# Performance work log

Measured on AMD Instinct MI355X. Metric: run time of the kernel, lower is better.

## Reference

```python
import jax, jax.numpy as jnp
import numpy as np

B, D = 8192, 1024            # batch, inputs_dim
H1, H2, H3 = 2048, 1024, 512 # expert_units
NS, NT = 8, 4                # num_shared_experts, num_tasks_experts
E = NS + 3 * NT              # 20 experts total: [shared 0:8 | SA 8:12 | RA 12:16 | EA 16:20]
TU1, TU2 = 1024, 512         # tower_units
TIN = H3 * 4                 # tower input dim = 2048


def lrelu(x):
    return jnp.where(x >= 0, x, 0.1 * x)


def setup_inputs() -> dict:
    key = jax.random.key(0)
    ks = jax.random.split(key, 24)
    s = 0.02
    return {
        "inputs": jax.random.normal(ks[0], (B, D), jnp.float32),
        # stacked expert MLP params (leading axis = expert index)
        "W1": jax.random.normal(ks[1], (E, D, H1), jnp.float32) * s,
        "b1": jnp.zeros((E, H1), jnp.float32),
        "W2": jax.random.normal(ks[2], (E, H1, H2), jnp.float32) * s,
        "b2": jnp.zeros((E, H2), jnp.float32),
        "W3": jax.random.normal(ks[3], (E, H2, H3), jnp.float32) * s,
        "b3": jnp.zeros((E, H3), jnp.float32),
        # gate linears (single layer + softmax over dim 1)
        "Wg_sh": jax.random.normal(ks[4], (D, NS + 3 * NT), jnp.float32) * s,
        "bg_sh": jnp.zeros((NS + 3 * NT,), jnp.float32),
        "Wg_sa": jax.random.normal(ks[5], (D, NT + NS), jnp.float32) * s,
        "bg_sa": jnp.zeros((NT + NS,), jnp.float32),
        "Wg_ra": jax.random.normal(ks[6], (D, NT + NS), jnp.float32) * s,
        "bg_ra": jnp.zeros((NT + NS,), jnp.float32),
        "Wg_ea": jax.random.normal(ks[7], (D, NT + NS), jnp.float32) * s,
        "bg_ea": jnp.zeros((NT + NS,), jnp.float32),
        # 2 towers (one per task), stacked on leading axis
        "Wt1": jax.random.normal(ks[8], (2, TIN, TU1), jnp.float32) * s,
        "bt1": jnp.zeros((2, TU1), jnp.float32),
        "Wt2": jax.random.normal(ks[9], (2, TU1, TU2), jnp.float32) * s,
        "bt2": jnp.zeros((2, TU2), jnp.float32),
        # per-task output denses: PRESENCE=6, AIRFLOW=4
        "Wd0": jax.random.normal(ks[10], (TU2, 6), jnp.float32) * s,
        "bd0": jnp.zeros((6,), jnp.float32),
        "Wd1": jax.random.normal(ks[11], (TU2, 4), jnp.float32) * s,
        "bd1": jnp.zeros((4,), jnp.float32),
    }


def reference(inputs, W1, b1, W2, b2, W3, b3,
              Wg_sh, bg_sh, Wg_sa, bg_sa, Wg_ra, bg_ra, Wg_ea, bg_ea,
              Wt1, bt1, Wt2, bt2, Wd0, bd0, Wd1, bd1):
    x = inputs
    # all 20 experts as batched GEMMs: [E, B, h]
    h = lrelu(jnp.einsum('bd,edh->ebh', x, W1) + b1[:, None, :])
    h = lrelu(jnp.einsum('ebh,ehk->ebk', h, W2) + b2[:, None, :])
    eo = lrelu(jnp.einsum('ebk,eko->ebo', h, W3) + b3[:, None, :])  # [E,B,H3]

    # gates (softmax over feature dim)
    g_sh = jax.nn.softmax(x @ Wg_sh + bg_sh, axis=1)  # [B, 20]
    g_sa = jax.nn.softmax(x @ Wg_sa + bg_sa, axis=1)  # [B, 12]
    g_ra = jax.nn.softmax(x @ Wg_ra + bg_ra, axis=1)
    g_ea = jax.nn.softmax(x @ Wg_ea + bg_ea, axis=1)

    # shared gate: order = shared + SA + RA + EA == natural stacking order
    out_sh = jnp.einsum('ebh,be->bh', eo, g_sh)
    # task gates: order = task experts + shared experts
    out_sa = jnp.einsum('ebh,be->bh', jnp.concatenate([eo[NS:NS+NT], eo[:NS]], 0), g_sa)
    out_ra = jnp.einsum('ebh,be->bh', jnp.concatenate([eo[NS+NT:NS+2*NT], eo[:NS]], 0), g_ra)
    out_ea = jnp.einsum('ebh,be->bh', jnp.concatenate([eo[NS+2*NT:], eo[:NS]], 0), g_ea)

    tower_in = jnp.concatenate([out_sh, out_sa, out_ra, out_ea], axis=1)  # [B, 2048]
    t = lrelu(jnp.einsum('bi,kio->kbo', tower_in, Wt1) + bt1[:, None, :])  # [2,B,TU1]
    t = lrelu(jnp.einsum('kbo,kop->kbp', t, Wt2) + bt2[:, None, :])        # [2,B,TU2]
    out0 = t[0] @ Wd0 + bd0  # [B, 6]  PRESENCE
    out1 = t[1] @ Wd1 + bd1  # [B, 4]  AIRFLOW
    return (out0, out1)
```

## Files before the change

kernel.cpp:

```cpp
#include <hip/hip_runtime.h>

#define DEV __device__ __forceinline__

typedef __bf16 bf16x8 __attribute__((ext_vector_type(8)));
typedef float f32x4 __attribute__((ext_vector_type(4)));

DEV unsigned short f2bf(float f) {
  union { float f; unsigned u; } v; v.f = f;
  unsigned r = v.u + 0x7FFFu + ((v.u >> 16) & 1u);
  return (unsigned short)(r >> 16);
}
DEV float bf2f(unsigned short h) {
  union { float f; unsigned u; } v; v.u = ((unsigned)h) << 16;
  return v.f;
}

DEV void gload16(const void* g, void* l) {
  __builtin_amdgcn_global_load_lds(
      (__attribute__((address_space(1))) void*)(g),
      (__attribute__((address_space(3))) void*)(l), 16, 0, 0);
}

#define MFMA16(a, b, c) __builtin_amdgcn_mfma_f32_16x16x32_bf16((a), (b), (c), 0, 0, 0)

DEV void gemm256_body(
    const unsigned short* __restrict__ A,
    const unsigned short* __restrict__ Bt,
    const float* __restrict__ bias,
    unsigned short* __restrict__ Out,
    int K, int lda, int ldo, int nbx, int nby,
    long sA, long sB, long sBias, long sOut,
    int bid, int nwg)
{
  int wg = bid;
  {
    const int q = nwg >> 3, r = nwg & 7;
    const int xcd = wg & 7, pos = wg >> 3;
    wg = (xcd < r ? xcd * (q + 1) : r * (q + 1) + (xcd - r) * q) + pos;
  }
  const int per_z = nbx * nby;
  const int z  = wg / per_z;
  const int rz = wg - z * per_z;
  const int by = rz / nbx;
  const int bx = rz - by * nbx;

  A    += (size_t)z * sA;
  Bt   += (size_t)z * sB;
  bias += (size_t)z * sBias;
  Out  += (size_t)z * sOut;

  const int tid  = threadIdx.x;
  const int lane = tid & 63;
  const int wid  = tid >> 6;
  const int wm   = wid >> 2, wn = wid & 3;
  const int m0   = by * 256, n0 = bx * 256;

  __shared__ alignas(16) char sm[2][65536];

  f32x4 acc[8][4];
  const f32x4 fz = {0.f, 0.f, 0.f, 0.f};
#pragma unroll
  for (int i = 0; i < 8; ++i)
#pragma unroll
    for (int j = 0; j < 4; ++j) acc[i][j] = fz;

  const int rr = tid >> 3;
  const int ch = (tid & 7) ^ (rr & 7);
  const char* gA = (const char*)A  + ((size_t)(m0 + rr) * lda) * 2 + ch * 16;
  const char* gB = (const char*)Bt + ((size_t)(n0 + rr) * K)   * 2 + ch * 16;
  const size_t stepA = (size_t)64 * lda * 2;
  const size_t stepB = (size_t)64 * K * 2;

  const int koff0 = (((lane >> 4) << 4) ^ ((lane & 7) << 4));
  const int aRow  = wm * 128 + (lane & 15);
  const int bRow  = wn * 64  + (lane & 15);

  const int nkt = K >> 6;

  auto SA = [&](int buf, int kt, int jh) {
    const char* s = gA + (size_t)kt * 128 + (2 * jh) * stepA;
    char* l = sm[buf] + tid * 16 + (2 * jh) * 8192;
    gload16(s, l);
    gload16(s + stepA, l + 8192);
  };
  auto SB = [&](int buf, int kt, int jh) {
    const char* s = gB + (size_t)kt * 128 + (2 * jh) * stepB;
    char* l = sm[buf] + 32768 + tid * 16 + (2 * jh) * 8192;
    gload16(s, l);
    gload16(s + stepB, l + 8192);
  };

  SA(0, 0, 0); SA(0, 0, 1); SB(0, 0, 0); SB(0, 0, 1);

  for (int kt = 0; kt < nkt; ++kt) {
    const int cur = kt & 1, nb = cur ^ 1;
    const bool pre = (kt + 1 < nkt);
    if (pre) {
      SA(nb, kt + 1, 0);
      asm volatile("s_waitcnt vmcnt(2)" ::: "memory");
    } else {
      asm volatile("s_waitcnt vmcnt(0)" ::: "memory");
    }
    __builtin_amdgcn_s_barrier();
    __builtin_amdgcn_sched_barrier(0);

    const char* pA = sm[cur] + aRow * 128;
    const char* pB = sm[cur] + 32768 + bRow * 128;
    bf16x8 a0[4], a1[4], b0[4], b1[4];

    {
#pragma unroll
      for (int i = 0; i < 4; ++i) a0[i] = *(const bf16x8*)(pA + i * 2048 + koff0);
#pragma unroll
      for (int n = 0; n < 4; ++n) b0[n] = *(const bf16x8*)(pB + n * 2048 + koff0);
      if (pre) SA(nb, kt + 1, 1);
      asm volatile("s_waitcnt lgkmcnt(0)" ::: "memory");
      __builtin_amdgcn_sched_barrier(0);
      __builtin_amdgcn_s_setprio(1);
#pragma unroll
      for (int i = 0; i < 4; ++i)
#pragma unroll
        for (int n = 0; n < 4; ++n) acc[i][n] = MFMA16(a0[i], b0[n], acc[i][n]);
      __builtin_amdgcn_s_setprio(0);
      __builtin_amdgcn_sched_barrier(0);
      __builtin_amdgcn_s_barrier();
      __builtin_amdgcn_sched_barrier(0);
    }
    {
#pragma unroll
      for (int i = 0; i < 4; ++i) a1[i] = *(const bf16x8*)(pA + (i + 4) * 2048 + koff0);
      if (pre) { SB(nb, kt + 1, 0); SB(nb, kt + 1, 1); }
      asm volatile("s_waitcnt lgkmcnt(0)" ::: "memory");
      __builtin_amdgcn_sched_barrier(0);
      __builtin_amdgcn_s_setprio(1);
#pragma unroll
      for (int i = 0; i < 4; ++i)
#pragma unroll
        for (int n = 0; n < 4; ++n) acc[i + 4][n] = MFMA16(a1[i], b0[n], acc[i + 4][n]);
      __builtin_amdgcn_s_setprio(0);
      __builtin_amdgcn_sched_barrier(0);
      __builtin_amdgcn_s_barrier();
      __builtin_amdgcn_sched_barrier(0);
    }
    {
      const int ko = koff0 ^ 64;
#pragma unroll
      for (int i = 0; i < 4; ++i) a0[i] = *(const bf16x8*)(pA + i * 2048 + ko);
#pragma unroll
      for (int n = 0; n < 4; ++n) b1[n] = *(const bf16x8*)(pB + n * 2048 + ko);
      asm volatile("s_waitcnt lgkmcnt(0)" ::: "memory");
      __builtin_amdgcn_sched_barrier(0);
      __builtin_amdgcn_s_setprio(1);
#pragma unroll
      for (int i = 0; i < 4; ++i)
#pragma unroll
        for (int n = 0; n < 4; ++n) acc[i][n] = MFMA16(a0[i], b1[n], acc[i][n]);
      __builtin_amdgcn_s_setprio(0);
      __builtin_amdgcn_sched_barrier(0);
      __builtin_amdgcn_s_barrier();
      __builtin_amdgcn_sched_barrier(0);
    }
    {
      const int ko = koff0 ^ 64;
#pragma unroll
      for (int i = 0; i < 4; ++i) a1[i] = *(const bf16x8*)(pA + (i + 4) * 2048 + ko);
      asm volatile("s_waitcnt lgkmcnt(0)" ::: "memory");
      __builtin_amdgcn_sched_barrier(0);
      __builtin_amdgcn_s_setprio(1);
#pragma unroll
      for (int i = 0; i < 4; ++i)
#pragma unroll
        for (int n = 0; n < 4; ++n) acc[i + 4][n] = MFMA16(a1[i], b1[n], acc[i + 4][n]);
      __builtin_amdgcn_s_setprio(0);
      __builtin_amdgcn_sched_barrier(0);
      __builtin_amdgcn_s_barrier();
      __builtin_amdgcn_sched_barrier(0);
    }
  }

#pragma unroll
  for (int ni = 0; ni < 4; ++ni) {
    const int c = n0 + wn * 64 + ni * 16 + (lane & 15);
    const float bv = bias[c];
#pragma unroll
    for (int mi = 0; mi < 8; ++mi) {
      const int r0 = m0 + wm * 128 + mi * 16 + ((lane >> 4) << 2);
#pragma unroll
      for (int j = 0; j < 4; ++j) {
        float v = acc[mi][ni][j] + bv;
        v = v >= 0.f ? v : 0.1f * v;
        Out[(size_t)(r0 + j) * ldo + c] = f2bf(v);
      }
    }
  }
}

__global__ __launch_bounds__(512) void gemm_dual(
    const unsigned short* A1, const unsigned short* Bt1, const float* bias1,
    unsigned short* O1, int K1, int lda1, int ldo1, int nbx1, int nby1,
    long sA1, long sB1, long sBias1, long sO1,
    const unsigned short* A2, const unsigned short* Bt2, const float* bias2,
    unsigned short* O2, int K2, int lda2, int ldo2, int nbx2, int nby2,
    long sA2, long sB2, long sBias2, long sO2,
    int split)
{
  const bool one = ((int)blockIdx.x < split);
  const unsigned short* A  = one ? A1 : A2;
  const unsigned short* Bt = one ? Bt1 : Bt2;
  const float* bias        = one ? bias1 : bias2;
  unsigned short* Out      = one ? O1 : O2;
  const int K   = one ? K1 : K2;
  const int lda = one ? lda1 : lda2;
  const int ldo = one ? ldo1 : ldo2;
  const int nbx = one ? nbx1 : nbx2;
  const int nby = one ? nby1 : nby2;
  const long sA = one ? sA1 : sA2;
  const long sB = one ? sB1 : sB2;
  const long sBias = one ? sBias1 : sBias2;
  const long sOut  = one ? sO1 : sO2;
  const int bid = one ? (int)blockIdx.x : (int)blockIdx.x - split;
  const int nwg = one ? split : (int)gridDim.x - split;
  gemm256_body(A, Bt, bias, Out, K, lda, ldo, nbx, nby, sA, sB, sBias, sOut,
               bid, nwg);
}

#define GEMM_DEF(NAME)                                                        \
__global__ __launch_bounds__(512) void NAME(                                  \
    const unsigned short* __restrict__ A,                                     \
    const unsigned short* __restrict__ Bt,                                    \
    const float* __restrict__ bias,                                           \
    unsigned short* __restrict__ Out,                                         \
    int K, int lda, int ldo, int nbx, int nby,                                \
    long sA, long sB, long sBias, long sOut) {                                \
  gemm256_body(A, Bt, bias, Out, K, lda, ldo, nbx, nby, sA, sB, sBias, sOut,  \
               (int)blockIdx.x, (int)gridDim.x);                              \
}
GEMM_DEF(gemm_l3)
GEMM_DEF(gemm_tw)

DEV float gateW(const float* Wsh, const float* Wsa, const float* Wra,
                const float* Wea, int k, int c) {
  if (c < 20) return Wsh[(size_t)k * 20 + c];
  if (c < 32) return Wsa[(size_t)k * 12 + (c - 20)];
  if (c < 44) return Wra[(size_t)k * 12 + (c - 32)];
  if (c < 56) return Wea[(size_t)k * 12 + (c - 44)];
  return 0.f;
}
DEV float gateB(const float* bsh, const float* bsa, const float* bra,
                const float* bea, int c) {
  if (c < 20) return bsh[c];
  if (c < 32) return bsa[c - 20];
  if (c < 44) return bra[c - 32];
  if (c < 56) return bea[c - 44];
  return 0.f;
}

__global__ __launch_bounds__(256) void prep_all(
    const float* __restrict__ W1,  const float* __restrict__ W2,
    const float* __restrict__ W3,  const float* __restrict__ Wt1,
    const float* __restrict__ Wt2, const float* __restrict__ x,
    const float* __restrict__ Wsh, const float* __restrict__ bsh,
    const float* __restrict__ Wsa, const float* __restrict__ bsa,
    const float* __restrict__ Wra, const float* __restrict__ bra,
    const float* __restrict__ Wea, const float* __restrict__ bea,
    unsigned short* __restrict__ W1t,  unsigned short* __restrict__ W2t,
    unsigned short* __restrict__ W3t,  unsigned short* __restrict__ Wt1t,
    unsigned short* __restrict__ Wt2t, unsigned short* __restrict__ xb,
    float* __restrict__ logits)
{
  const int id = blockIdx.x;
  const int t  = threadIdx.x;

  if (id < 128) {
    __shared__ alignas(16) float smg[4096];
    float (*sx)[64] = (float (*)[64])smg;
    float (*sw)[64] = (float (*)[64])(smg + 2048);
    const int b0 = id * 64;
    const int tr = t >> 4, tc = t & 15;
    float acc[4][4] = {};

    for (int kt = 0; kt < 32; ++kt) {
      const int k0 = kt * 32;
      __syncthreads();
#pragma unroll
      for (int it = 0; it < 2; ++it) {
        const int idx = t + it * 256;
        const int r = idx >> 3, c4 = (idx & 7) * 4;
        const float4 v = *(const float4*)(x + (size_t)(b0 + r) * 1024 + k0 + c4);
        sx[c4 + 0][r] = v.x; sx[c4 + 1][r] = v.y;
        sx[c4 + 2][r] = v.z; sx[c4 + 3][r] = v.w;
      }
#pragma unroll
      for (int it = 0; it < 2; ++it) {
        const int idx = t + it * 256;
        const int row = idx >> 4;
        const int c4  = (idx & 15) * 4;
#pragma unroll
        for (int j = 0; j < 4; ++j)
          sw[row][c4 + j] = gateW(Wsh, Wsa, Wra, Wea, k0 + row, c4 + j);
      }
      __syncthreads();
#pragma unroll
      for (int kk = 0; kk < 32; ++kk) {
        const float4 rx = *(const float4*)&sx[kk][tr * 4];
        const float4 wv = *(const float4*)&sw[kk][tc * 4];
#pragma unroll
        for (int i = 0; i < 4; ++i) {
          const float xv = (i == 0) ? rx.x : (i == 1) ? rx.y : (i == 2) ? rx.z : rx.w;
          acc[i][0] += xv * wv.x; acc[i][1] += xv * wv.y;
          acc[i][2] += xv * wv.z; acc[i][3] += xv * wv.w;
        }
      }
    }
    float bv[4];
#pragma unroll
    for (int j = 0; j < 4; ++j) bv[j] = gateB(bsh, bsa, bra, bea, tc * 4 + j);
#pragma unroll
    for (int i = 0; i < 4; ++i) {
      float4 o;
      o.x = acc[i][0] + bv[0]; o.y = acc[i][1] + bv[1];
      o.z = acc[i][2] + bv[2]; o.w = acc[i][3] + bv[3];
      *(float4*)&logits[(size_t)(b0 + tr * 4 + i) * 64 + tc * 4] = o;
    }
    return;
  }

  if (id >= 24448) {
    const int local = id - 24448;
    const int r0 = (local >> 4) * 64, c0 = (local & 15) * 64;
#pragma unroll
    for (int i = 0; i < 4; ++i) {
      const int row = r0 + i * 16 + (t >> 4);
      const int col = c0 + (t & 15) * 4;
      const float4 v = *(const float4*)(x + (size_t)row * 1024 + col);
      ushort4 u = make_ushort4(f2bf(v.x), f2bf(v.y), f2bf(v.z), f2bf(v.w));
      *(ushort4*)(xb + (size_t)row * 1024 + col) = u;
    }
    return;
  }

  const int g = id - 128;
  const float* src; unsigned short* dst; int K, N, local;
  if (g < 10240)      { src = W1;  dst = W1t;  K = 1024; N = 2048; local = g; }
  else if (g < 20480) { src = W2;  dst = W2t;  K = 2048; N = 1024; local = g - 10240; }
  else if (g < 23040) { src = W3;  dst = W3t;  K = 1024; N = 512;  local = g - 20480; }
  else if (g < 24064) { src = Wt1; dst = Wt1t; K = 2048; N = 1024; local = g - 23040; }
  else                { src = Wt2; dst = Wt2t; K = 1024; N = 512;  local = g - 24064; }

  const int nkt = K >> 6, nnt = N >> 6;
  const int per_z = nkt * nnt;
  const int z   = local / per_z;
  const int rem = local - z * per_z;
  const int k0  = (rem % nkt) * 64;
  const int n0  = (rem / nkt) * 64;
  src += (size_t)z * K * N;
  dst += (size_t)z * K * N;

  const int i4 = (t >> 4) * 4;
  const int j4 = (t & 15) * 4;
  float a[4][4];
#pragma unroll
  for (int rr = 0; rr < 4; ++rr)
    *(float4*)a[rr] = *(const float4*)(src + (size_t)(k0 + i4 + rr) * N + n0 + j4);
#pragma unroll
  for (int c = 0; c < 4; ++c) {
    ushort4 u = make_ushort4(f2bf(a[0][c]), f2bf(a[1][c]),
                             f2bf(a[2][c]), f2bf(a[3][c]));
    *(ushort4*)(dst + (size_t)(n0 + j4 + c) * K + k0 + i4) = u;
  }
}

__global__ __launch_bounds__(256) void combine_k(
    const unsigned short* __restrict__ eo,
    const float* __restrict__ logits,
    unsigned short* __restrict__ tin)
{
  const int b = blockIdx.x;
  const int t = threadIdx.x;
  __shared__ alignas(16) unsigned short lds[20][512];
  __shared__ float gsm[56];
  const unsigned short* er = eo + (size_t)b * 10240;
  unsigned short* ldsf = &lds[0][0];
#pragma unroll
  for (int i = 0; i < 5; ++i)
    gload16(er + (i * 256 + t) * 8, ldsf + (i * 256 + t) * 8);

  if (t < 64) {
    const float v0 = (t < 56) ? logits[(size_t)b * 64 + t] : 0.f;
    const int off[4] = {0, 20, 32, 44};
    const int wd[4]  = {20, 12, 12, 12};
    for (int g = 0; g < 4; ++g) {
      const bool in = (t >= off[g]) && (t < off[g] + wd[g]);
      float vv = in ? v0 : -1e30f;
      float m = vv;
#pragma unroll
      for (int o = 32; o; o >>= 1) m = fmaxf(m, __shfl_xor(m, o));
      float e = in ? __expf(vv - m) : 0.f;
      float s = e;
#pragma unroll
      for (int o = 32; o; o >>= 1) s += __shfl_xor(s, o);
      if (in) gsm[t] = e / s;
    }
  }
  __syncthreads();

  const int sec = t >> 6;
  const int h0 = (t & 63) * 8;
  float acc[8] = {0.f, 0.f, 0.f, 0.f, 0.f, 0.f, 0.f, 0.f};
  if (sec == 0) {
    for (int e = 0; e < 20; ++e) {
      const float w = gsm[e];
#pragma unroll
      for (int j = 0; j < 8; ++j) acc[j] += w * bf2f(lds[e][h0 + j]);
    }
  } else {
    const int goff = 20 + (sec - 1) * 12;
    const int ebase = 8 + (sec - 1) * 4;
    for (int tt = 0; tt < 4; ++tt) {
      const float w = gsm[goff + tt];
#pragma unroll
      for (int j = 0; j < 8; ++j) acc[j] += w * bf2f(lds[ebase + tt][h0 + j]);
    }
    for (int ss = 0; ss < 8; ++ss) {
      const float w = gsm[goff + 4 + ss];
#pragma unroll
      for (int j = 0; j < 8; ++j) acc[j] += w * bf2f(lds[ss][h0 + j]);
    }
  }
  unsigned short* ob = tin + (size_t)b * 2048 + sec * 512 + h0;
  ushort4 u0 = make_ushort4(f2bf(acc[0]), f2bf(acc[1]), f2bf(acc[2]), f2bf(acc[3]));
  ushort4 u1 = make_ushort4(f2bf(acc[4]), f2bf(acc[5]), f2bf(acc[6]), f2bf(acc[7]));
  *(ushort4*)ob = u0;
  *(ushort4*)(ob + 4) = u1;
}

__global__ __launch_bounds__(256) void outd_k(
    const unsigned short* __restrict__ t2,
    const float* __restrict__ Wd0, const float* __restrict__ bd0,
    const float* __restrict__ Wd1, const float* __restrict__ bd1,
    float* __restrict__ out)
{
  const int gid = blockIdx.x * 4 + (threadIdx.x >> 6);
  const int lane = threadIdx.x & 63;
  const int b = gid >> 1, task = gid & 1;
  const uint4 raw = *(const uint4*)(t2 + ((size_t)task * 8192 + b) * 512 + lane * 8);
  const unsigned short* rs = (const unsigned short*)&raw;
  float v[8];
#pragma unroll
  for (int j = 0; j < 8; ++j) v[j] = bf2f(rs[j]);
  const float* Wd = task ? Wd1 : Wd0;
  const float* bd = task ? bd1 : bd0;
  const int ncol = task ? 4 : 6;
  float* ob = task ? (out + (size_t)8192 * 6 + (size_t)b * 4) : (out + (size_t)b * 6);
  for (int c = 0; c < ncol; ++c) {
    float p = 0.f;
#pragma unroll
    for (int j = 0; j < 8; ++j) p += v[j] * Wd[(size_t)(lane * 8 + j) * ncol + c];
#pragma unroll
    for (int o = 32; o; o >>= 1) p += __shfl_xor(p, o);
    if (lane == 0) ob[c] = p + bd[c];
  }
}

extern "C" void kernel_launch(void* const* d_in, const int* in_sizes, int n_in,
                              void* d_out, int out_size, void* d_ws, size_t ws_size,
                              hipStream_t stream) {
  const float* x     = (const float*)d_in[0];
  const float* W1    = (const float*)d_in[1];
  const float* b1    = (const float*)d_in[2];
  const float* W2    = (const float*)d_in[3];
  const float* b2    = (const float*)d_in[4];
  const float* W3    = (const float*)d_in[5];
  const float* b3    = (const float*)d_in[6];
  const float* Wg_sh = (const float*)d_in[7];
  const float* bg_sh = (const float*)d_in[8];
  const float* Wg_sa = (const float*)d_in[9];
  const float* bg_sa = (const float*)d_in[10];
  const float* Wg_ra = (const float*)d_in[11];
  const float* bg_ra = (const float*)d_in[12];
  const float* Wg_ea = (const float*)d_in[13];
  const float* bg_ea = (const float*)d_in[14];
  const float* Wt1   = (const float*)d_in[15];
  const float* bt1   = (const float*)d_in[16];
  const float* Wt2   = (const float*)d_in[17];
  const float* bt2   = (const float*)d_in[18];
  const float* Wd0   = (const float*)d_in[19];
  const float* bd0   = (const float*)d_in[20];
  const float* Wd1   = (const float*)d_in[21];
  const float* bd1   = (const float*)d_in[22];
  float* out = (float*)d_out;

  const int B = 8192, D = 1024, H1 = 2048, H2 = 1024, H3 = 512;
  const int E = 20, TU1 = 1024, TU2 = 512, TIN = 2048;

  auto rnd = [](size_t n) { return (n + 255) & ~(size_t)255; };
  const size_t szTin = rnd((size_t)B * TIN * 2);
  const size_t szT1  = rnd((size_t)2 * B * TU1 * 2);
  const size_t szH1e = rnd((size_t)B * H1 * 2);
  const size_t szH2e = rnd((size_t)B * H2 * 2);

  char* w = (char*)d_ws;
  auto alloc = [&](size_t n) { char* p = w; w += rnd(n); return p; };
  unsigned short* xb   = (unsigned short*)alloc((size_t)B * D * 2);
  unsigned short* W1t  = (unsigned short*)alloc((size_t)E * H1 * D * 2);
  unsigned short* W2t  = (unsigned short*)alloc((size_t)E * H2 * H1 * 2);
  unsigned short* W3t  = (unsigned short*)alloc((size_t)E * H3 * H2 * 2);
  unsigned short* Wt1t = (unsigned short*)alloc((size_t)2 * TU1 * TIN * 2);
  unsigned short* Wt2t = (unsigned short*)alloc((size_t)2 * TU2 * TU1 * 2);
  float*          lgts = (float*)alloc((size_t)B * 64 * 4);
  unsigned short* eo   = (unsigned short*)alloc((size_t)E * B * H3 * 2);
  char* hreg = w;
  unsigned short* h1  = (unsigned short*)hreg;
  unsigned short* h2  = (unsigned short*)(hreg + 4 * szH1e);
  unsigned short* tin = (unsigned short*)hreg;
  unsigned short* t1  = (unsigned short*)(hreg + szTin);
  unsigned short* t2  = (unsigned short*)(hreg + szTin + szT1);
  (void)in_sizes; (void)n_in; (void)out_size; (void)ws_size;

  prep_all<<<dim3(26496), 256, 0, stream>>>(
      W1, W2, W3, Wt1, Wt2, x,
      Wg_sh, bg_sh, Wg_sa, bg_sa, Wg_ra, bg_ra, Wg_ea, bg_ea,
      W1t, W2t, W3t, Wt1t, Wt2t, xb, lgts);

  for (int k = 0; k <= 10; ++k) {
    const bool has1 = (k < 10), has2 = (k > 0);
    const int split = has1 ? 512 : 0;
    const int total = split + (has2 ? 256 : 0);
    const int p1 = k, p2 = k - 1;
    const unsigned short* A1 = xb;
    const unsigned short* B1 = W1t + (size_t)(2 * (has1 ? p1 : 0)) * H1 * D;
    const float* bb1 = b1 + (size_t)(2 * (has1 ? p1 : 0)) * H1;
    unsigned short* O1 = h1 + (size_t)((has1 ? p1 : 0) & 1) * 2 * B * H1;
    const unsigned short* A2 = h1 + (size_t)((has2 ? p2 : 0) & 1) * 2 * B * H1;
    const unsigned short* B2 = W2t + (size_t)(2 * (has2 ? p2 : 0)) * H2 * H1;
    const float* bb2 = b2 + (size_t)(2 * (has2 ? p2 : 0)) * H2;
    unsigned short* O2 = h2 + (size_t)((2 * (has2 ? p2 : 0)) & 3) * B * H2;
    gemm_dual<<<dim3(total), 512, 0, stream>>>(
        A1, B1, bb1, O1, D, D, H1, H1 / 256, B / 256,
        0, (long)H1 * D, (long)H1, (long)B * H1,
        A2, B2, bb2, O2, H1, H1, H2, H2 / 256, B / 256,
        (long)B * H1, (long)H2 * H1, (long)H2, (long)B * H2,
        split);
    if (k >= 2 && (k & 1) == 0) {
      const int w2 = (k - 2) / 2;
      gemm_l3<<<dim3((H3 / 256) * (B / 256) * 4), 512, 0, stream>>>(
          h2, W3t + (size_t)(4 * w2) * H3 * H2, b3 + (size_t)(4 * w2) * H3,
          eo + (size_t)(4 * w2) * H3,
          H2, H2, E * H3, H3 / 256, B / 256,
          (long)B * H2, (long)H3 * H2, (long)H3, (long)H3);
    }
  }

  combine_k<<<dim3(B), 256, 0, stream>>>(eo, lgts, tin);

  gemm_tw<<<dim3((TU1 / 256) * (B / 256) * 2), 512, 0, stream>>>(
      tin, Wt1t, bt1, t1, TIN, TIN, TU1, TU1 / 256, B / 256,
      0, (long)TU1 * TIN, (long)TU1, (long)B * TU1);
  gemm_tw<<<dim3((TU2 / 256) * (B / 256) * 2), 512, 0, stream>>>(
      t1, Wt2t, bt2, t2, TU1, TU1, TU2, TU2 / 256, B / 256,
      (long)B * TU1, (long)TU2 * TU1, (long)TU2, (long)B * TU2);

  outd_k<<<dim3(B * 2 / 4), 256, 0, stream>>>(t2, Wd0, bd0, Wd1, bd1, out);
}
```

Baseline: 2.064 ms.

## Make GEMM kernels persistent and prefetch next tile's first stage during epilogue

Turns the 256x256 GEMM body into a persistent loop: the grid is capped at 256 workgroups (one per CU) and each workgroup walks tiles with stride gridDim. The first k-stage of the next tile is loaded into LDS before the current tile's epilogue stores, so that load latency hides behind the output writes. This removes per-workgroup launch and prologue cost and tail effects, but changes the XCD tile-swizzle mapping because tile indices are now decoded per iteration. It also adds serialization within each CU, since a second workgroup can no longer co-reside to hide stalls.

After: 2.047 ms. No clear change (-0.8%).

```diff
diff --git a/kernel.cpp b/kernel.cpp
--- a/kernel.cpp
+++ b/kernel.cpp
@@ -23,14 +23,19 @@
 
 #define MFMA16(a, b, c) __builtin_amdgcn_mfma_f32_16x16x32_bf16((a), (b), (c), 0, 0, 0)
 
-DEV void gemm256_body(
-    const unsigned short* __restrict__ A,
-    const unsigned short* __restrict__ Bt,
-    const float* __restrict__ bias,
-    unsigned short* __restrict__ Out,
-    int K, int lda, int ldo, int nbx, int nby,
-    long sA, long sB, long sBias, long sOut,
-    int bid, int nwg)
+struct TileCtx {
+  const char* gA;
+  const char* gB;
+  size_t stepA, stepB;
+  const float* bias;
+  unsigned short* Out;
+  int nkt, ldo, n0, m0;
+};
+
+DEV TileCtx tile_decode(int bid, int nwg,
+    const unsigned short* A, const unsigned short* Bt, const float* bias,
+    unsigned short* Out, int K, int lda, int ldo, int nbx, int nby,
+    long sA, long sB, long sBias, long sOut, int rr, int ch)
 {
   int wg = bid;
   {
@@ -44,154 +49,190 @@
   const int by = rz / nbx;
   const int bx = rz - by * nbx;
 
-  A    += (size_t)z * sA;
-  Bt   += (size_t)z * sB;
-  bias += (size_t)z * sBias;
-  Out  += (size_t)z * sOut;
+  TileCtx c;
+  c.nkt = K >> 6;
+  c.ldo = ldo;
+  c.m0  = by * 256;
+  c.n0  = bx * 256;
+  c.bias = bias + (size_t)z * sBias;
+  c.Out  = Out  + (size_t)z * sOut;
+  c.gA = (const char*)(A  + (size_t)z * sA) + ((size_t)(c.m0 + rr) * lda) * 2 + ch * 16;
+  c.gB = (const char*)(Bt + (size_t)z * sB) + ((size_t)(c.n0 + rr) * K)   * 2 + ch * 16;
+  c.stepA = (size_t)64 * lda * 2;
+  c.stepB = (size_t)64 * K * 2;
+  return c;
+}
+
+DEV void gemm_persist(
+    const unsigned short* A1, const unsigned short* Bt1, const float* bias1,
+    unsigned short* O1, int K1, int lda1, int ldo1, int nbx1, int nby1,
+    long sA1, long sB1, long sBias1, long sO1,
+    const unsigned short* A2, const unsigned short* Bt2, const float* bias2,
+    unsigned short* O2, int K2, int lda2, int ldo2, int nbx2, int nby2,
+    long sA2, long sB2, long sBias2, long sO2,
+    int split, int total)
+{
+  __shared__ alignas(16) char sm[2][65536];
+  char* smb = &sm[0][0];
 
   const int tid  = threadIdx.x;
   const int lane = tid & 63;
   const int wid  = tid >> 6;
   const int wm   = wid >> 2, wn = wid & 3;
-  const int m0   = by * 256, n0 = bx * 256;
-
-  __shared__ alignas(16) char sm[2][65536];
-
-  f32x4 acc[8][4];
-  const f32x4 fz = {0.f, 0.f, 0.f, 0.f};
-#pragma unroll
-  for (int i = 0; i < 8; ++i)
-#pragma unroll
-    for (int j = 0; j < 4; ++j) acc[i][j] = fz;
-
   const int rr = tid >> 3;
   const int ch = (tid & 7) ^ (rr & 7);
-  const char* gA = (const char*)A  + ((size_t)(m0 + rr) * lda) * 2 + ch * 16;
-  const char* gB = (const char*)Bt + ((size_t)(n0 + rr) * K)   * 2 + ch * 16;
-  const size_t stepA = (size_t)64 * lda * 2;
-  const size_t stepB = (size_t)64 * K * 2;
-
   const int koff0 = (((lane >> 4) << 4) ^ ((lane & 7) << 4));
   const int aRow  = wm * 128 + (lane & 15);
   const int bRow  = wn * 64  + (lane & 15);
 
-  const int nkt = K >> 6;
-
-  auto SA = [&](int buf, int kt, int jh) {
-    const char* s = gA + (size_t)kt * 128 + (2 * jh) * stepA;
-    char* l = sm[buf] + tid * 16 + (2 * jh) * 8192;
+  auto dec = [&](int tix) -> TileCtx {
+    if (tix < split)
+      return tile_decode(tix, split, A1, Bt1, bias1, O1, K1, lda1, ldo1,
+                         nbx1, nby1, sA1, sB1, sBias1, sO1, rr, ch);
+    return tile_decode(tix - split, total - split, A2, Bt2, bias2, O2, K2,
+                       lda2, ldo2, nbx2, nby2, sA2, sB2, sBias2, sO2, rr, ch);
+  };
+  auto SA = [&](const TileCtx& c, int buf, int kt, int jh) {
+    const char* s = c.gA + (size_t)kt * 128 + (2 * jh) * c.stepA;
+    char* l = smb + buf * 65536 + tid * 16 + (2 * jh) * 8192;
     gload16(s, l);
-    gload16(s + stepA, l + 8192);
+    gload16(s + c.stepA, l + 8192);
   };
-  auto SB = [&](int buf, int kt, int jh) {
-    const char* s = gB + (size_t)kt * 128 + (2 * jh) * stepB;
-    char* l = sm[buf] + 32768 + tid * 16 + (2 * jh) * 8192;
+  auto SB = [&](const TileCtx& c, int buf, int kt, int jh) {
+    const char* s = c.gB + (size_t)kt * 128 + (2 * jh) * c.stepB;
+    char* l = smb + buf * 65536 + 32768 + tid * 16 + (2 * jh) * 8192;
     gload16(s, l);
-    gload16(s + stepB, l + 8192);
+    gload16(s + c.stepB, l + 8192);
   };
-
-  SA(0, 0, 0); SA(0, 0, 1); SB(0, 0, 0); SB(0, 0, 1);
-
-  for (int kt = 0; kt < nkt; ++kt) {
-    const int cur = kt & 1, nb = cur ^ 1;
-    const bool pre = (kt + 1 < nkt);
-    if (pre) {
-      SA(nb, kt + 1, 0);
-      asm volatile("s_waitcnt vmcnt(2)" ::: "memory");
-    } else {
-      asm volatile("s_waitcnt vmcnt(0)" ::: "memory");
-    }
-    __builtin_amdgcn_s_barrier();
-    __builtin_amdgcn_sched_barrier(0);
-
-    const char* pA = sm[cur] + aRow * 128;
-    const char* pB = sm[cur] + 32768 + bRow * 128;
-    bf16x8 a0[4], a1[4], b0[4], b1[4];
-
-    {
-#pragma unroll
-      for (int i = 0; i < 4; ++i) a0[i] = *(const bf16x8*)(pA + i * 2048 + koff0);
-#pragma unroll
-      for (int n = 0; n < 4; ++n) b0[n] = *(const bf16x8*)(pB + n * 2048 + koff0);
-      if (pre) SA(nb, kt + 1, 1);
-      asm volatile("s_waitcnt lgkmcnt(0)" ::: "memory");
-      __builtin_amdgcn_sched_barrier(0);
-      __builtin_amdgcn_s_setprio(1);
-#pragma unroll
-      for (int i = 0; i < 4; ++i)
-#pragma unroll
-        for (int n = 0; n < 4; ++n) acc[i][n] = MFMA16(a0[i], b0[n], acc[i][n]);
-      __builtin_amdgcn_s_setprio(0);
-      __builtin_amdgcn_sched_barrier(0);
+  auto STAGE0 = [&](const TileCtx& c) {
+    SA(c, 0, 0, 0); SA(c, 0, 0, 1); SB(c, 0, 0, 0); SB(c, 0, 0, 1);
+  };
+
+  int tix = (int)blockIdx.x;
+  if (tix >= total) return;
+  TileCtx cur = dec(tix);
+  STAGE0(cur);
+
+  f32x4 acc[8][4];
+  const f32x4 fz = {0.f, 0.f, 0.f, 0.f};
+
+  while (true) {
+#pragma unroll
+    for (int i = 0; i < 8; ++i)
+#pragma unroll
+      for (int j = 0; j < 4; ++j) acc[i][j] = fz;
+
+    const int nkt = cur.nkt;
+    for (int kt = 0; kt < nkt; ++kt) {
+      const int cb = kt & 1, nb = cb ^ 1;
+      const bool pre = (kt + 1 < nkt);
+      if (pre) {
+        SA(cur, nb, kt + 1, 0);
+        asm volatile("s_waitcnt vmcnt(2)" ::: "memory");
+      } else {
+        asm volatile("s_waitcnt vmcnt(0)" ::: "memory");
+      }
       __builtin_amdgcn_s_barrier();
       __builtin_amdgcn_sched_barrier(0);
-    }
-    {
-#pragma unroll
-      for (int i = 0; i < 4; ++i) a1[i] = *(const bf16x8*)(pA + (i + 4) * 2048 + koff0);
-      if (pre) { SB(nb, kt + 1, 0); SB(nb, kt + 1, 1); }
-      asm volatile("s_waitcnt lgkmcnt(0)" ::: "memory");
-      __builtin_amdgcn_sched_barrier(0);
-      __builtin_amdgcn_s_setprio(1);
-#pragma unroll
-      for (int i = 0; i < 4; ++i)
-#pragma unroll
-        for (int n = 0; n < 4; ++n) acc[i + 4][n] = MFMA16(a1[i], b0[n], acc[i + 4][n]);
-      __builtin_amdgcn_s_setprio(0);
-      __builtin_amdgcn_sched_barrier(0);
-      __builtin_amdgcn_s_barrier();
-      __builtin_amdgcn_sched_barrier(0);
-    }
-    {
-      const int ko = koff0 ^ 64;
-#pragma unroll
-      for (int i = 0; i < 4; ++i) a0[i] = *(const bf16x8*)(pA + i * 2048 + ko);
-#pragma unroll
-      for (int n = 0; n < 4; ++n) b1[n] = *(const bf16x8*)(pB + n * 2048 + ko);
-      asm volatile("s_waitcnt lgkmcnt(0)" ::: "memory");
-      __builtin_amdgcn_sched_barrier(0);
-      __builtin_amdgcn_s_setprio(1);
-#pragma unroll
-      for (int i = 0; i < 4; ++i)
-#pragma unroll
-        for (int n = 0; n < 4; ++n) acc[i][n] = MFMA16(a0[i], b1[n], acc[i][n]);
-      __builtin_amdgcn_s_setprio(0);
-      __builtin_amdgcn_sched_barrier(0);
-      __builtin_amdgcn_s_barrier();
-      __builtin_amdgcn_sched_barrier(0);
-    }
-    {
-      const int ko = koff0 ^ 64;
-#pragma unroll
-      for (int i = 0; i < 4; ++i) a1[i] = *(const bf16x8*)(pA + (i + 4) * 2048 + ko);
-      asm volatile("s_waitcnt lgkmcnt(0)" ::: "memory");
-      __builtin_amdgcn_sched_barrier(0);
-      __builtin_amdgcn_s_setprio(1);
-#pragma unroll
-      for (int i = 0; i < 4; ++i)
-#pragma unroll
-        for (int n = 0; n < 4; ++n) acc[i + 4][n] = MFMA16(a1[i], b1[n], acc[i + 4][n]);
-      __builtin_amdgcn_s_setprio(0);
-      __builtin_amdgcn_sched_barrier(0);
-      __builtin_amdgcn_s_barrier();
-      __builtin_amdgcn_sched_barrier(0);
-    }
-  }
-
-#pragma unroll
-  for (int ni = 0; ni < 4; ++ni) {
-    const int c = n0 + wn * 64 + ni * 16 + (lane & 15);
-    const float bv = bias[c];
-#pragma unroll
-    for (int mi = 0; mi < 8; ++mi) {
-      const int r0 = m0 + wm * 128 + mi * 16 + ((lane >> 4) << 2);
-#pragma unroll
-      for (int j = 0; j < 4; ++j) {
-        float v = acc[mi][ni][j] + bv;
-        v = v >= 0.f ? v : 0.1f * v;
-        Out[(size_t)(r0 + j) * ldo + c] = f2bf(v);
-      }
-    }
+
+      const char* pA = smb + cb * 65536 + aRow * 128;
+      const char* pB = smb + cb * 65536 + 32768 + bRow * 128;
+      bf16x8 a0[4], a1[4], b0[4], b1[4];
+
+      {
+#pragma unroll
+        for (int i = 0; i < 4; ++i) a0[i] = *(const bf16x8*)(pA + i * 2048 + koff0);
+#pragma unroll
+        for (int n = 0; n < 4; ++n) b0[n] = *(const bf16x8*)(pB + n * 2048 + koff0);
+        if (pre) SA(cur, nb, kt + 1, 1);
+        asm volatile("s_waitcnt lgkmcnt(0)" ::: "memory");
+        __builtin_amdgcn_sched_barrier(0);
+        __builtin_amdgcn_s_setprio(1);
+#pragma unroll
+        for (int i = 0; i < 4; ++i)
+#pragma unroll
+          for (int n = 0; n < 4; ++n) acc[i][n] = MFMA16(a0[i], b0[n], acc[i][n]);
+        __builtin_amdgcn_s_setprio(0);
+        __builtin_amdgcn_sched_barrier(0);
+        __builtin_amdgcn_s_barrier();
+        __builtin_amdgcn_sched_barrier(0);
+      }
+      {
+#pragma unroll
+        for (int i = 0; i < 4; ++i) a1[i] = *(const bf16x8*)(pA + (i + 4) * 2048 + koff0);
+        if (pre) { SB(cur, nb, kt + 1, 0); SB(cur, nb, kt + 1, 1); }
+        asm volatile("s_waitcnt lgkmcnt(0)" ::: "memory");
+        __builtin_amdgcn_sched_barrier(0);
+        __builtin_amdgcn_s_setprio(1);
+#pragma unroll
+        for (int i = 0; i < 4; ++i)
+#pragma unroll
+          for (int n = 0; n < 4; ++n) acc[i + 4][n] = MFMA16(a1[i], b0[n], acc[i + 4][n]);
+        __builtin_amdgcn_s_setprio(0);
+        __builtin_amdgcn_sched_barrier(0);
+        __builtin_amdgcn_s_barrier();
+        __builtin_amdgcn_sched_barrier(0);
+      }
+      {
+        const int ko = koff0 ^ 64;
+#pragma unroll
+        for (int i = 0; i < 4; ++i) a0[i] = *(const bf16x8*)(pA + i * 2048 + ko);
+#pragma unroll
+        for (int n = 0; n < 4; ++n) b1[n] = *(const bf16x8*)(pB + n * 2048 + ko);
+        asm volatile("s_waitcnt lgkmcnt(0)" ::: "memory");
+        __builtin_amdgcn_sched_barrier(0);
+        __builtin_amdgcn_s_setprio(1);
+#pragma unroll
+        for (int i = 0; i < 4; ++i)
+#pragma unroll
+          for (int n = 0; n < 4; ++n) acc[i][n] = MFMA16(a0[i], b1[n], acc[i][n]);
+        __builtin_amdgcn_s_setprio(0);
+        __builtin_amdgcn_sched_barrier(0);
+        __builtin_amdgcn_s_barrier();
+        __builtin_amdgcn_sched_barrier(0);
+      }
+      {
+        const int ko = koff0 ^ 64;
+#pragma unroll
+        for (int i = 0; i < 4; ++i) a1[i] = *(const bf16x8*)(pA + (i + 4) * 2048 + ko);
+        asm volatile("s_waitcnt lgkmcnt(0)" ::: "memory");
+        __builtin_amdgcn_sched_barrier(0);
+        __builtin_amdgcn_s_setprio(1);
+#pragma unroll
+        for (int i = 0; i < 4; ++i)
+#pragma unroll
+          for (int n = 0; n < 4; ++n) acc[i + 4][n] = MFMA16(a1[i], b1[n], acc[i + 4][n]);
+        __builtin_amdgcn_s_setprio(0);
+        __builtin_amdgcn_sched_barrier(0);
+        __builtin_amdgcn_s_barrier();
+        __builtin_amdgcn_sched_barrier(0);
+      }
+    }
+
+    const int nxt = tix + (int)gridDim.x;
+    const bool has = nxt < total;
+    TileCtx nc;
+    if (has) { nc = dec(nxt); STAGE0(nc); }
+
+#pragma unroll
+    for (int ni = 0; ni < 4; ++ni) {
+      const int c = cur.n0 + wn * 64 + ni * 16 + (lane & 15);
+      const float bv = cur.bias[c];
+#pragma unroll
+      for (int mi = 0; mi < 8; ++mi) {
+        const int r0 = cur.m0 + wm * 128 + mi * 16 + ((lane >> 4) << 2);
+#pragma unroll
+        for (int j = 0; j < 4; ++j) {
+          float v = acc[mi][ni][j] + bv;
+          v = v >= 0.f ? v : 0.1f * v;
+          cur.Out[(size_t)(r0 + j) * cur.ldo + c] = f2bf(v);
+        }
+      }
+    }
+
+    if (!has) return;
+    cur = nc;
+    tix = nxt;
   }
 }
 
@@ -202,38 +243,22 @@
     const unsigned short* A2, const unsigned short* Bt2, const float* bias2,
     unsigned short* O2, int K2, int lda2, int ldo2, int nbx2, int nby2,
     long sA2, long sB2, long sBias2, long sO2,
-    int split)
+    int split, int total)
 {
-  const bool one = ((int)blockIdx.x < split);
-  const unsigned short* A  = one ? A1 : A2;
-  const unsigned short* Bt = one ? Bt1 : Bt2;
-  const float* bias        = one ? bias1 : bias2;
-  unsigned short* Out      = one ? O1 : O2;
-  const int K   = one ? K1 : K2;
-  const int lda = one ? lda1 : lda2;
-  const int ldo = one ? ldo1 : ldo2;
-  const int nbx = one ? nbx1 : nbx2;
-  const int nby = one ? nby1 : nby2;
-  const long sA = one ? sA1 : sA2;
-  const long sB = one ? sB1 : sB2;
-  const long sBias = one ? sBias1 : sBias2;
-  const long sOut  = one ? sO1 : sO2;
-  const int bid = one ? (int)blockIdx.x : (int)blockIdx.x - split;
-  const int nwg = one ? split : (int)gridDim.x - split;
-  gemm256_body(A, Bt, bias, Out, K, lda, ldo, nbx, nby, sA, sB, sBias, sOut,
-               bid, nwg);
+  gemm_persist(A1, Bt1, bias1, O1, K1, lda1, ldo1, nbx1, nby1,
+               sA1, sB1, sBias1, sO1,
+               A2, Bt2, bias2, O2, K2, lda2, ldo2, nbx2, nby2,
+               sA2, sB2, sBias2, sO2, split, total);
 }
 
 #define GEMM_DEF(NAME)                                                        \
 __global__ __launch_bounds__(512) void NAME(                                  \
-    const unsigned short* __restrict__ A,                                     \
-    const unsigned short* __restrict__ Bt,                                    \
-    const float* __restrict__ bias,                                           \
-    unsigned short* __restrict__ Out,                                         \
-    int K, int lda, int ldo, int nbx, int nby,                                \
-    long sA, long sB, long sBias, long sOut) {                                \
-  gemm256_body(A, Bt, bias, Out, K, lda, ldo, nbx, nby, sA, sB, sBias, sOut,  \
-               (int)blockIdx.x, (int)gridDim.x);                              \
+    const unsigned short* A, const unsigned short* Bt, const float* bias,     \
+    unsigned short* Out, int K, int lda, int ldo, int nbx, int nby,           \
+    long sA, long sB, long sBias, long sOut, int total) {                     \
+  gemm_persist(A, Bt, bias, Out, K, lda, ldo, nbx, nby, sA, sB, sBias, sOut,  \
+               A, Bt, bias, Out, K, lda, ldo, nbx, nby, sA, sB, sBias, sOut,  \
+               total, total);                                                 \
 }
 GEMM_DEF(gemm_l3)
 GEMM_DEF(gemm_tw)
@@ -497,7 +522,6 @@
   const size_t szTin = rnd((size_t)B * TIN * 2);
   const size_t szT1  = rnd((size_t)2 * B * TU1 * 2);
   const size_t szH1e = rnd((size_t)B * H1 * 2);
-  const size_t szH2e = rnd((size_t)B * H2 * 2);
 
   char* w = (char*)d_ws;
   auto alloc = [&](size_t n) { char* p = w; w += rnd(n); return p; };
@@ -535,30 +559,31 @@
     const unsigned short* B2 = W2t + (size_t)(2 * (has2 ? p2 : 0)) * H2 * H1;
     const float* bb2 = b2 + (size_t)(2 * (has2 ? p2 : 0)) * H2;
     unsigned short* O2 = h2 + (size_t)((2 * (has2 ? p2 : 0)) & 3) * B * H2;
-    gemm_dual<<<dim3(total), 512, 0, stream>>>(
+    const int grid = total < 256 ? total : 256;
+    gemm_dual<<<dim3(grid), 512, 0, stream>>>(
         A1, B1, bb1, O1, D, D, H1, H1 / 256, B / 256,
         0, (long)H1 * D, (long)H1, (long)B * H1,
         A2, B2, bb2, O2, H1, H1, H2, H2 / 256, B / 256,
         (long)B * H1, (long)H2 * H1, (long)H2, (long)B * H2,
-        split);
+        split, total);
     if (k >= 2 && (k & 1) == 0) {
       const int w2 = (k - 2) / 2;
-      gemm_l3<<<dim3((H3 / 256) * (B / 256) * 4), 512, 0, stream>>>(
+      gemm_l3<<<dim3(256), 512, 0, stream>>>(
           h2, W3t + (size_t)(4 * w2) * H3 * H2, b3 + (size_t)(4 * w2) * H3,
           eo + (size_t)(4 * w2) * H3,
           H2, H2, E * H3, H3 / 256, B / 256,
-          (long)B * H2, (long)H3 * H2, (long)H3, (long)H3);
+          (long)B * H2, (long)H3 * H2, (long)H3, (long)H3, 256);
     }
   }
 
   combine_k<<<dim3(B), 256, 0, stream>>>(eo, lgts, tin);
 
-  gemm_tw<<<dim3((TU1 / 256) * (B / 256) * 2), 512, 0, stream>>>(
+  gemm_tw<<<dim3(256), 512, 0, stream>>>(
       tin, Wt1t, bt1, t1, TIN, TIN, TU1, TU1 / 256, B / 256,
-      0, (long)TU1 * TIN, (long)TU1, (long)B * TU1);
-  gemm_tw<<<dim3((TU2 / 256) * (B / 256) * 2), 512, 0, stream>>>(
+      0, (long)TU1 * TIN, (long)TU1, (long)B * TU1, 256);
+  gemm_tw<<<dim3(128), 512, 0, stream>>>(
       t1, Wt2t, bt2, t2, TU1, TU1, TU2, TU2 / 256, B / 256,
-      (long)B * TU1, (long)TU2 * TU1, (long)TU2, (long)B * TU2);
+      (long)B * TU1, (long)TU2 * TU1, (long)TU2, (long)B * TU2, 128);
 
   outd_k<<<dim3(B * 2 / 4), 256, 0, stream>>>(t2, Wd0, bd0, Wd1, bd1, out);
 }
```
